# Kernel tuning notes

Hardware: AMD Instinct MI355X
Metric: run time of the kernel (lower is better)

Reference implementation:

```python
import jax, jax.numpy as jnp
import numpy as np

B = 4096
D = 2048
K = 8          # num_intention
H2 = 64        # fc2 out


def setup_inputs() -> dict:
    key = jax.random.key(0)
    ks = jax.random.split(key, 8)
    x = jax.random.normal(ks[0], (B, D), dtype=jnp.float32)
    # one-hot intention per sample
    idx = jax.random.randint(ks[1], (B,), 0, K)
    intention = jax.nn.one_hot(idx, K, dtype=jnp.float32)
    s1 = 1.0 / np.sqrt(D)
    s2 = 1.0 / np.sqrt(K)
    s3 = 1.0 / np.sqrt(D + H2)
    W1 = jax.random.uniform(ks[2], (D * K, D), jnp.float32, -s1, s1)
    b1 = jax.random.uniform(ks[3], (D * K,), jnp.float32, -s1, s1)
    W2 = jax.random.uniform(ks[4], (H2, K), jnp.float32, -s2, s2)
    b2 = jax.random.uniform(ks[5], (H2,), jnp.float32, -s2, s2)
    W3 = jax.random.uniform(ks[6], (1, D + H2), jnp.float32, -s3, s3)
    b3 = jax.random.uniform(ks[7], (1,), jnp.float32, -s3, s3)
    return {"x": x, "intention": intention, "W1": W1, "b1": b1,
            "W2": W2, "b2": b2, "W3": W3, "b3": b3}


def reference(x, intention, W1, b1, W2, b2, W3, b3):
    # fc2 on the one-hot intention -> [B, 64]
    y2 = intention @ W2.T + b2
    # fc1 densely computes all K branches (dropout treated as identity / eval mode)
    y1 = x @ W1.T + b1                      # [B, D*K]
    # mask = intention.repeat(1, 2048): branch axis is INNERMOST (interleaved)
    y1 = y1.reshape(B, D, K)                # [B, D, K]
    sel = jax.lax.stop_gradient(intention)  # mask is non-differentiable in torch
    y1 = jnp.einsum('bdk,bk->bd', y1, sel)  # gather active branch -> [B, D]
    y3 = jax.nn.relu(jnp.concatenate([y1, y2], axis=1))  # [B, D+64]
    y = y3 @ W3.T + b3                      # [B, 1]
    return y
```

## Files before the change

kernel.cpp:

```cpp
#include <hip/hip_runtime.h>
#include <hip/hip_bf16.h>
#include <stdint.h>

#define NB 4096
#define ND 2048
#define NK 8
#define NH 64

#define BM 128
#define BN 128
#define BK 32
#define MAX_ROWS 5120
#define MAX_TILES 40

#define CONV_BLOCKS  (NK * ND)
#define XCONV_BLOCKS NB
#define KIDX_BLOCKS  (NB / 256)
#define PREP_GRID    (CONV_BLOCKS + XCONV_BLOCKS + KIDX_BLOCKS)

typedef __bf16 bf16;
typedef __bf16 bf16x8 __attribute__((ext_vector_type(8)));
typedef float floatx4 __attribute__((ext_vector_type(4)));

#define OFF_KIDX   0u
#define OFF_ORDER  16384u
#define OFF_META   40960u
#define OFF_CUR    41472u
#define OFF_C2S    41536u
#define OFF_CNTP   41600u
#define OFF_XC     65536u
#define OFF_WB     16842752u

__device__ inline void cvt_row16(const float* __restrict__ src, bf16* __restrict__ dst) {
    float4 a = *(const float4*)(src);
    float4 c = *(const float4*)(src + 4);
    bf16x8 v;
    v[0] = (bf16)a.x; v[1] = (bf16)a.y; v[2] = (bf16)a.z; v[3] = (bf16)a.w;
    v[4] = (bf16)c.x; v[5] = (bf16)c.y; v[6] = (bf16)c.z; v[7] = (bf16)c.w;
    *(bf16x8*)dst = v;
}

__global__ void __launch_bounds__(256)
prep_conv_kernel(const float* __restrict__ x,
                 const float* __restrict__ intention,
                 const float* __restrict__ W1,
                 int* __restrict__ kidx,
                 int* __restrict__ cntp,
                 bf16* __restrict__ xc,
                 bf16* __restrict__ Wb)
{
    const int blk = blockIdx.x;
    const int tid = threadIdx.x;

    if (blk < CONV_BLOCKS) {
        const int d = blk >> 3;
        const int k = blk & 7;
        cvt_row16(W1 + (size_t)blk * ND + tid * 8,
                  Wb + ((size_t)k * ND + d) * ND + tid * 8);
    } else if (blk < CONV_BLOCKS + XCONV_BLOCKS) {
        const int row = blk - CONV_BLOCKS;
        cvt_row16(x + (size_t)row * ND + tid * 8,
                  xc + (size_t)row * ND + tid * 8);
    } else {
        __shared__ int h[NK];
        const int hb = blk - CONV_BLOCKS - XCONV_BLOCKS;
        if (tid < NK) h[tid] = 0;
        __syncthreads();
        const int b = hb * 256 + tid;
        float4 a = *(const float4*)(intention + (size_t)b * NK);
        float4 c = *(const float4*)(intention + (size_t)b * NK + 4);
        int k = 0;
        if (a.y > 0.5f) k = 1;
        if (a.z > 0.5f) k = 2;
        if (a.w > 0.5f) k = 3;
        if (c.x > 0.5f) k = 4;
        if (c.y > 0.5f) k = 5;
        if (c.z > 0.5f) k = 6;
        if (c.w > 0.5f) k = 7;
        kidx[b] = k;
        atomicAdd(&h[k], 1);
        __syncthreads();
        if (tid < NK) cntp[hb * NK + tid] = h[tid];
    }
}

__global__ void __launch_bounds__(256)
meta_kernel(const int* __restrict__ cntp,
            const float* __restrict__ W2,
            const float* __restrict__ b2,
            const float* __restrict__ W3,
            const float* __restrict__ b3,
            int* __restrict__ meta,
            int* __restrict__ cursors,
            float* __restrict__ c2s)
{
    __shared__ int cnt[NK];
    const int tid = threadIdx.x;
    if (tid < NK) {
        int s = 0;
#pragma unroll
        for (int i = 0; i < KIDX_BLOCKS; i++) s += cntp[i * NK + tid];
        cnt[tid] = s;
    }
    if (tid >= 64 && tid < 128) {
        const int l = tid - 64;
        const int k = l & 7;
        const int hc = l >> 3;
        float s = 0.f;
#pragma unroll
        for (int j = 0; j < 8; j++) {
            int h = hc * 8 + j;
            float v = W2[h * NK + k] + b2[h];
            if (v > 0.f) s += v * W3[ND + h];
        }
        s += __shfl_xor(s, 8, 64);
        s += __shfl_xor(s, 16, 64);
        s += __shfl_xor(s, 32, 64);
        if (l < 8) c2s[k] = s + b3[0];
    }
    __syncthreads();
    if (tid == 0) {
        int running = 0, nt = 0;
        for (int k = 0; k < NK; k++) {
            cursors[k] = running;
            int ntile = (cnt[k] + BM - 1) / BM;
            for (int t = 0; t < ntile && nt < MAX_TILES; t++) {
                meta[1 + nt] = k;
                meta[1 + MAX_TILES + nt] = running + t * BM;
                nt++;
            }
            running += ntile * BM;
        }
        meta[0] = nt;
    }
}

__global__ void __launch_bounds__(256)
scatter_kernel(const int* __restrict__ kidx,
               int* __restrict__ cursors,
               const float* __restrict__ c2s,
               int* __restrict__ order,
               float* __restrict__ out)
{
    const int b = blockIdx.x * 256 + threadIdx.x;
    const int lane = threadIdx.x & 63;
    const int k = kidx[b] & 7;
    out[b] = c2s[k];

    const unsigned long long below = (lane == 63) ? ~0ull >> 1
                                   : ((1ull << lane) - 1);
    int pos = 0;
#pragma unroll
    for (int kk = 0; kk < NK; kk++) {
        unsigned long long m = __ballot(k == kk);
        if (m) {
            int leader = __ffsll((long long)m) - 1;
            int base = 0;
            if (lane == leader) base = atomicAdd(&cursors[kk], __popcll(m));
            base = __shfl(base, leader, 64);
            if (k == kk) pos = base + __popcll(m & below);
        }
    }
    if (pos >= 0 && pos < MAX_ROWS) order[pos] = b;
}

__global__ void __launch_bounds__(256)
gemm_kernel(const bf16* __restrict__ xc,
            const bf16* __restrict__ Wb,
            const int* __restrict__ order,
            const int* __restrict__ meta,
            const float* __restrict__ b1,
            const float* __restrict__ W3,
            float* __restrict__ out)
{
    int n_mt = meta[0];
    if (n_mt > MAX_TILES) n_mt = MAX_TILES;
    const int mt = blockIdx.y;
    if (mt >= n_mt) return;
    const int kbr = meta[1 + mt] & 7;
    int row0 = meta[1 + MAX_TILES + mt];
    if (row0 < 0) row0 = 0;
    if (row0 > MAX_ROWS - BM) row0 = MAX_ROWS - BM;
    const int col0 = blockIdx.x * BN;

    __shared__ bf16 As[BM * BK];
    __shared__ bf16 Bs[BN * BK];
    __shared__ int rowb[BM];

    const int tid = threadIdx.x;
    const int lane = tid & 63;
    const int wid = tid >> 6;
    const int wm = wid >> 1;
    const int wn = wid & 1;

    if (tid < BM) {
        int b = order[row0 + tid];
        rowb[tid] = (b >= 0 && b < NB) ? b : -1;
    }
    __syncthreads();

    const int srow = tid >> 2;
    const int scol = (tid & 3) * 8;
    const int ra0 = rowb[srow];
    const int ra1 = rowb[64 + srow];
    const bf16* pa0 = xc + (size_t)(ra0 < 0 ? 0 : ra0) * ND + scol;
    const bf16* pa1 = xc + (size_t)(ra1 < 0 ? 0 : ra1) * ND + scol;
    const bf16* pb0 = Wb + ((size_t)kbr * ND + col0 + srow) * ND + scol;
    const bf16* pb1 = pb0 + (size_t)64 * ND;
    bf16* la0 = As + wid * 512;
    bf16* la1 = As + 2048 + wid * 512;
    bf16* lb0 = Bs + wid * 512;
    bf16* lb1 = Bs + 2048 + wid * 512;

    floatx4 zero = {0.f, 0.f, 0.f, 0.f};
    floatx4 acc[4][4];
#pragma unroll
    for (int i = 0; i < 4; i++)
#pragma unroll
        for (int j = 0; j < 4; j++) acc[i][j] = zero;

    const int qk = (lane >> 4) * 8;
    const int mrow = lane & 15;

    for (int kk = 0; kk < ND; kk += BK) {
        __builtin_amdgcn_global_load_lds(
            (const __attribute__((address_space(1))) void*)(pa0 + kk),
            (__attribute__((address_space(3))) void*)la0, 16, 0, 0);
        __builtin_amdgcn_global_load_lds(
            (const __attribute__((address_space(1))) void*)(pa1 + kk),
            (__attribute__((address_space(3))) void*)la1, 16, 0, 0);
        __builtin_amdgcn_global_load_lds(
            (const __attribute__((address_space(1))) void*)(pb0 + kk),
            (__attribute__((address_space(3))) void*)lb0, 16, 0, 0);
        __builtin_amdgcn_global_load_lds(
            (const __attribute__((address_space(1))) void*)(pb1 + kk),
            (__attribute__((address_space(3))) void*)lb1, 16, 0, 0);
        __syncthreads();

        bf16x8 af[4], bfv[4];
#pragma unroll
        for (int i = 0; i < 4; i++) {
            af[i]  = *(const bf16x8*)(As + (wm * 64 + i * 16 + mrow) * BK + qk);
            bfv[i] = *(const bf16x8*)(Bs + (wn * 64 + i * 16 + mrow) * BK + qk);
        }
#pragma unroll
        for (int i = 0; i < 4; i++)
#pragma unroll
            for (int j = 0; j < 4; j++)
                acc[i][j] = __builtin_amdgcn_mfma_f32_16x16x32_bf16(
                    af[i], bfv[j], acc[i][j], 0, 0, 0);
        __syncthreads();
    }

    const int colq = lane & 15;
    const int quad = lane >> 4;
    float bias[4], w3v[4];
#pragma unroll
    for (int j = 0; j < 4; j++) {
        int d = col0 + wn * 64 + j * 16 + colq;
        bias[j] = b1[d * NK + kbr];
        w3v[j] = W3[d];
    }
#pragma unroll
    for (int i = 0; i < 4; i++) {
#pragma unroll
        for (int r = 0; r < 4; r++) {
            float s = 0.f;
#pragma unroll
            for (int j = 0; j < 4; j++) {
                float v = acc[i][j][r] + bias[j];
                s += (v > 0.f) ? v * w3v[j] : 0.f;
            }
#pragma unroll
            for (int m = 1; m < 16; m <<= 1) s += __shfl_xor(s, m, 64);
            if (colq == 0) {
                int b = rowb[wm * 64 + i * 16 + quad * 4 + r];
                if (b >= 0) atomicAdd(out + b, s);
            }
        }
    }
}

extern "C" void kernel_launch(void* const* d_in, const int* in_sizes, int n_in,
                              void* d_out, int out_size, void* d_ws, size_t ws_size,
                              hipStream_t stream)
{
    const float* x         = (const float*)d_in[0];
    const float* intention = (const float*)d_in[1];
    const float* W1        = (const float*)d_in[2];
    const float* b1        = (const float*)d_in[3];
    const float* W2        = (const float*)d_in[4];
    const float* b2        = (const float*)d_in[5];
    const float* W3        = (const float*)d_in[6];
    const float* b3        = (const float*)d_in[7];
    float* out = (float*)d_out;

    char* ws = (char*)d_ws;
    int*   kidx    = (int*)(ws + OFF_KIDX);
    int*   order   = (int*)(ws + OFF_ORDER);
    int*   meta    = (int*)(ws + OFF_META);
    int*   cursors = (int*)(ws + OFF_CUR);
    float* c2s     = (float*)(ws + OFF_C2S);
    int*   cntp    = (int*)(ws + OFF_CNTP);
    bf16*  xc      = (bf16*)(ws + OFF_XC);
    bf16*  Wb      = (bf16*)(ws + OFF_WB);

    prep_conv_kernel<<<dim3(PREP_GRID), dim3(256), 0, stream>>>(
        x, intention, W1, kidx, cntp, xc, Wb);
    meta_kernel<<<dim3(1), dim3(256), 0, stream>>>(
        cntp, W2, b2, W3, b3, meta, cursors, c2s);
    scatter_kernel<<<dim3(NB / 256), dim3(256), 0, stream>>>(
        kidx, cursors, c2s, order, out);
    gemm_kernel<<<dim3(ND / BN, MAX_TILES), dim3(256), 0, stream>>>(
        xc, Wb, order, meta, b1, W3, out);
}
```

Baseline: 315.3 us.

## Flatten fp32-to-bf16 conversion with nontemporal loads and keep W1 native row order

The prep kernel now converts W1 and x as flat contiguous streams of 16 elements per thread using nontemporal loads, with 2048 blocks instead of one block per row. W1 is no longer reordered into branch-major layout during conversion. The GEMM B-pointer indexing is changed to read the interleaved (d*K+k) row layout directly. This cuts prep launch overhead and scatter writes, but the GEMM tiles now read W1 rows strided by K rows, which may hurt locality.

After: 324.9 us. +3.0%, slower.

```diff
diff --git a/kernel.cpp b/kernel.cpp
--- a/kernel.cpp
+++ b/kernel.cpp
@@ -13,10 +13,10 @@
 #define MAX_ROWS 5120
 #define MAX_TILES 40
 
-#define CONV_BLOCKS  (NK * ND)
-#define XCONV_BLOCKS NB
+#define CONV_BLOCKS  2048
 #define KIDX_BLOCKS  (NB / 256)
-#define PREP_GRID    (CONV_BLOCKS + XCONV_BLOCKS + KIDX_BLOCKS)
+#define PREP_GRID    (CONV_BLOCKS + KIDX_BLOCKS)
+#define STRIPE 8388608
 
 typedef __bf16 bf16;
 typedef __bf16 bf16x8 __attribute__((ext_vector_type(8)));
@@ -31,13 +31,18 @@
 #define OFF_XC     65536u
 #define OFF_WB     16842752u
 
-__device__ inline void cvt_row16(const float* __restrict__ src, bf16* __restrict__ dst) {
-    float4 a = *(const float4*)(src);
-    float4 c = *(const float4*)(src + 4);
-    bf16x8 v;
-    v[0] = (bf16)a.x; v[1] = (bf16)a.y; v[2] = (bf16)a.z; v[3] = (bf16)a.w;
-    v[4] = (bf16)c.x; v[5] = (bf16)c.y; v[6] = (bf16)c.z; v[7] = (bf16)c.w;
-    *(bf16x8*)dst = v;
+__device__ inline void cvt16nt(const float* __restrict__ src, bf16* __restrict__ dst) {
+    floatx4 a = __builtin_nontemporal_load((const floatx4*)src);
+    floatx4 b = __builtin_nontemporal_load((const floatx4*)src + 1);
+    floatx4 c = __builtin_nontemporal_load((const floatx4*)src + 2);
+    floatx4 d = __builtin_nontemporal_load((const floatx4*)src + 3);
+    bf16x8 v0, v1;
+    v0[0] = (bf16)a[0]; v0[1] = (bf16)a[1]; v0[2] = (bf16)a[2]; v0[3] = (bf16)a[3];
+    v0[4] = (bf16)b[0]; v0[5] = (bf16)b[1]; v0[6] = (bf16)b[2]; v0[7] = (bf16)b[3];
+    v1[0] = (bf16)c[0]; v1[1] = (bf16)c[1]; v1[2] = (bf16)c[2]; v1[3] = (bf16)c[3];
+    v1[4] = (bf16)d[0]; v1[5] = (bf16)d[1]; v1[6] = (bf16)d[2]; v1[7] = (bf16)d[3];
+    *(bf16x8*)dst = v0;
+    *((bf16x8*)dst + 1) = v1;
 }
 
 __global__ void __launch_bounds__(256)
@@ -53,17 +58,14 @@
     const int tid = threadIdx.x;
 
     if (blk < CONV_BLOCKS) {
-        const int d = blk >> 3;
-        const int k = blk & 7;
-        cvt_row16(W1 + (size_t)blk * ND + tid * 8,
-                  Wb + ((size_t)k * ND + d) * ND + tid * 8);
-    } else if (blk < CONV_BLOCKS + XCONV_BLOCKS) {
-        const int row = blk - CONV_BLOCKS;
-        cvt_row16(x + (size_t)row * ND + tid * 8,
-                  xc + (size_t)row * ND + tid * 8);
+        const size_t t16 = ((size_t)blk * 256 + tid) * 16;
+#pragma unroll
+        for (int i = 0; i < 4; i++)
+            cvt16nt(W1 + (size_t)i * STRIPE + t16, Wb + (size_t)i * STRIPE + t16);
+        cvt16nt(x + t16, xc + t16);
     } else {
         __shared__ int h[NK];
-        const int hb = blk - CONV_BLOCKS - XCONV_BLOCKS;
+        const int hb = blk - CONV_BLOCKS;
         if (tid < NK) h[tid] = 0;
         __syncthreads();
         const int b = hb * 256 + tid;
@@ -205,8 +207,8 @@
     const int ra1 = rowb[64 + srow];
     const bf16* pa0 = xc + (size_t)(ra0 < 0 ? 0 : ra0) * ND + scol;
     const bf16* pa1 = xc + (size_t)(ra1 < 0 ? 0 : ra1) * ND + scol;
-    const bf16* pb0 = Wb + ((size_t)kbr * ND + col0 + srow) * ND + scol;
-    const bf16* pb1 = pb0 + (size_t)64 * ND;
+    const bf16* pb0 = Wb + ((size_t)(col0 + srow) * NK + kbr) * ND + scol;
+    const bf16* pb1 = pb0 + (size_t)64 * NK * ND;
     bf16* la0 = As + wid * 512;
     bf16* la1 = As + 2048 + wid * 512;
     bf16* lb0 = Bs + wid * 512;
```

## Fuse W1 fp32-to-bf16 conversion into GEMM B-tile loads, drop Wb prepass

Applied to the files above, without the earlier changes.

Removes the prep pass that converted all of W1 (128 MB fp32) to a branch-major bf16 copy. The GEMM now reads the fp32 W1 rows for its branch directly, converts them in registers and stores them to LDS. This avoids writing and re-reading a 64 MB bf16 weight buffer. In exchange the GEMM reads twice as many bytes for B per tile, gives up the async global-to-LDS path for B, and adds conversion work in the inner loop with no double buffering.

Result: no change. 318.0 us (+0.8%).

```diff
diff --git a/kernel.cpp b/kernel.cpp
--- a/kernel.cpp
+++ b/kernel.cpp
@@ -13,10 +13,9 @@
 #define MAX_ROWS 5120
 #define MAX_TILES 40
 
-#define CONV_BLOCKS  (NK * ND)
-#define XCONV_BLOCKS NB
+#define CONV_BLOCKS  4096
 #define KIDX_BLOCKS  (NB / 256)
-#define PREP_GRID    (CONV_BLOCKS + XCONV_BLOCKS + KIDX_BLOCKS)
+#define PREP_GRID    (CONV_BLOCKS + KIDX_BLOCKS)
 
 typedef __bf16 bf16;
 typedef __bf16 bf16x8 __attribute__((ext_vector_type(8)));
@@ -29,41 +28,32 @@
 #define OFF_C2S    41536u
 #define OFF_CNTP   41600u
 #define OFF_XC     65536u
-#define OFF_WB     16842752u
-
-__device__ inline void cvt_row16(const float* __restrict__ src, bf16* __restrict__ dst) {
+
+__device__ inline bf16x8 cvt8(const float* __restrict__ src) {
     float4 a = *(const float4*)(src);
     float4 c = *(const float4*)(src + 4);
     bf16x8 v;
     v[0] = (bf16)a.x; v[1] = (bf16)a.y; v[2] = (bf16)a.z; v[3] = (bf16)a.w;
     v[4] = (bf16)c.x; v[5] = (bf16)c.y; v[6] = (bf16)c.z; v[7] = (bf16)c.w;
-    *(bf16x8*)dst = v;
+    return v;
 }
 
 __global__ void __launch_bounds__(256)
 prep_conv_kernel(const float* __restrict__ x,
                  const float* __restrict__ intention,
-                 const float* __restrict__ W1,
                  int* __restrict__ kidx,
                  int* __restrict__ cntp,
-                 bf16* __restrict__ xc,
-                 bf16* __restrict__ Wb)
+                 bf16* __restrict__ xc)
 {
     const int blk = blockIdx.x;
     const int tid = threadIdx.x;
 
     if (blk < CONV_BLOCKS) {
-        const int d = blk >> 3;
-        const int k = blk & 7;
-        cvt_row16(W1 + (size_t)blk * ND + tid * 8,
-                  Wb + ((size_t)k * ND + d) * ND + tid * 8);
-    } else if (blk < CONV_BLOCKS + XCONV_BLOCKS) {
-        const int row = blk - CONV_BLOCKS;
-        cvt_row16(x + (size_t)row * ND + tid * 8,
-                  xc + (size_t)row * ND + tid * 8);
+        const size_t g = ((size_t)blk * 256 + tid) * 8;
+        *(bf16x8*)(xc + g) = cvt8(x + g);
     } else {
         __shared__ int h[NK];
-        const int hb = blk - CONV_BLOCKS - XCONV_BLOCKS;
+        const int hb = blk - CONV_BLOCKS;
         if (tid < NK) h[tid] = 0;
         __syncthreads();
         const int b = hb * 256 + tid;
@@ -166,7 +156,7 @@
 
 __global__ void __launch_bounds__(256)
 gemm_kernel(const bf16* __restrict__ xc,
-            const bf16* __restrict__ Wb,
+            const float* __restrict__ W1,
             const int* __restrict__ order,
             const int* __restrict__ meta,
             const float* __restrict__ b1,
@@ -205,12 +195,12 @@
     const int ra1 = rowb[64 + srow];
     const bf16* pa0 = xc + (size_t)(ra0 < 0 ? 0 : ra0) * ND + scol;
     const bf16* pa1 = xc + (size_t)(ra1 < 0 ? 0 : ra1) * ND + scol;
-    const bf16* pb0 = Wb + ((size_t)kbr * ND + col0 + srow) * ND + scol;
-    const bf16* pb1 = pb0 + (size_t)64 * ND;
+    const float* pw0 = W1 + ((size_t)(col0 + srow) * NK + kbr) * ND + scol;
+    const float* pw1 = pw0 + (size_t)64 * NK * ND;
     bf16* la0 = As + wid * 512;
     bf16* la1 = As + 2048 + wid * 512;
-    bf16* lb0 = Bs + wid * 512;
-    bf16* lb1 = Bs + 2048 + wid * 512;
+    bf16* lb0 = Bs + srow * BK + scol;
+    bf16* lb1 = Bs + (64 + srow) * BK + scol;
 
     floatx4 zero = {0.f, 0.f, 0.f, 0.f};
     floatx4 acc[4][4];
@@ -223,18 +213,23 @@
     const int mrow = lane & 15;
 
     for (int kk = 0; kk < ND; kk += BK) {
+        float4 b0a = *(const float4*)(pw0 + kk);
+        float4 b0b = *(const float4*)(pw0 + kk + 4);
+        float4 b1a = *(const float4*)(pw1 + kk);
+        float4 b1b = *(const float4*)(pw1 + kk + 4);
         __builtin_amdgcn_global_load_lds(
             (const __attribute__((address_space(1))) void*)(pa0 + kk),
             (__attribute__((address_space(3))) void*)la0, 16, 0, 0);
         __builtin_amdgcn_global_load_lds(
             (const __attribute__((address_space(1))) void*)(pa1 + kk),
             (__attribute__((address_space(3))) void*)la1, 16, 0, 0);
-        __builtin_amdgcn_global_load_lds(
-            (const __attribute__((address_space(1))) void*)(pb0 + kk),
-            (__attribute__((address_space(3))) void*)lb0, 16, 0, 0);
-        __builtin_amdgcn_global_load_lds(
-            (const __attribute__((address_space(1))) void*)(pb1 + kk),
-            (__attribute__((address_space(3))) void*)lb1, 16, 0, 0);
+        bf16x8 w0, w1;
+        w0[0] = (bf16)b0a.x; w0[1] = (bf16)b0a.y; w0[2] = (bf16)b0a.z; w0[3] = (bf16)b0a.w;
+        w0[4] = (bf16)b0b.x; w0[5] = (bf16)b0b.y; w0[6] = (bf16)b0b.z; w0[7] = (bf16)b0b.w;
+        w1[0] = (bf16)b1a.x; w1[1] = (bf16)b1a.y; w1[2] = (bf16)b1a.z; w1[3] = (bf16)b1a.w;
+        w1[4] = (bf16)b1b.x; w1[5] = (bf16)b1b.y; w1[6] = (bf16)b1b.z; w1[7] = (bf16)b1b.w;
+        *(bf16x8*)lb0 = w0;
+        *(bf16x8*)lb1 = w1;
         __syncthreads();
 
         bf16x8 af[4], bfv[4];
@@ -303,14 +298,13 @@
     float* c2s     = (float*)(ws + OFF_C2S);
     int*   cntp    = (int*)(ws + OFF_CNTP);
     bf16*  xc      = (bf16*)(ws + OFF_XC);
-    bf16*  Wb      = (bf16*)(ws + OFF_WB);
 
     prep_conv_kernel<<<dim3(PREP_GRID), dim3(256), 0, stream>>>(
-        x, intention, W1, kidx, cntp, xc, Wb);
+        x, intention, kidx, cntp, xc);
     meta_kernel<<<dim3(1), dim3(256), 0, stream>>>(
         cntp, W2, b2, W3, b3, meta, cursors, c2s);
     scatter_kernel<<<dim3(NB / 256), dim3(256), 0, stream>>>(
         kidx, cursors, c2s, order, out);
     gemm_kernel<<<dim3(ND / BN, MAX_TILES), dim3(256), 0, stream>>>(
-        xc, Wb, order, meta, b1, W3, out);
-}
+        xc, W1, order, meta, b1, W3, out);
+}
```
